# Kernel tuning notes

Measured on AMD Instinct MI355X. Metric: run time of the kernel, lower is better.

Reference implementation:

```python
import jax, jax.numpy as jnp
import numpy as np

GRID = 12  # sqrt(144), seq_len = 144 fixed by w_g shape


def _relative_position(n: int) -> jnp.ndarray:
    # grid cell centers for an n x n grid, flattened row-major -> (n*n,)
    idx = np.arange(n * n)
    row, col = idx // n, idx % n
    cx = (col + 0.5) / n  # (x_min + x_max)/2 with x_min=col/n, x_max=(col+1)/n
    cy = (row + 0.5) / n
    dx = cx[:, None] - cx[None, :]
    dy = cy[:, None] - cy[None, :]
    ax = np.sign(dx) * 0.5
    ay = np.sign(dy) * 0.5
    dx = np.abs(np.log(np.abs(dx) + 0.5))
    dy = np.abs(np.log(np.abs(dy) + 0.5))
    # cat along leading dim then permute(1,2,0) == stack last-dim in order (dx,dy,ax,ay)
    pos = np.stack([dx, dy, ax, ay], axis=-1).astype(np.float32)  # (S,S,4)
    return jnp.asarray(pos)


def setup_inputs() -> dict:
    key = jax.random.key(0)
    ks = jax.random.split(key, 9)
    B, S, D = 128, GRID * GRID, 1024
    sc = 1.0 / np.sqrt(D)
    return {
        "query": jax.random.normal(ks[0], (B, S, D), jnp.float32),
        "key": jax.random.normal(ks[1], (B, S, D), jnp.float32),
        "value": jax.random.normal(ks[2], (B, S, D), jnp.float32),
        "Wq": jax.random.normal(ks[3], (D, D), jnp.float32) * sc,
        "bq": jnp.zeros((D,), jnp.float32),
        "Wk": jax.random.normal(ks[4], (D, D), jnp.float32) * sc,
        "bk": jnp.zeros((D,), jnp.float32),
        "Wv": jax.random.normal(ks[5], (D, D), jnp.float32) * sc,
        "bv": jnp.zeros((D,), jnp.float32),
        "Wlin": jax.random.normal(ks[6], (D, 4), jnp.float32) * 0.5,
        "w_g": jax.random.normal(ks[7], (S, D, 1), jnp.float32) * sc,
    }


def reference(query, key, value, Wq, bq, Wk, bk, Wv, bv, Wlin, w_g):
    d_model = query.shape[-1]
    # QKV projections + ReLU activation (dropout is identity at eval)
    q = jax.nn.relu(jnp.einsum("bsd,ed->bse", query, Wq) + bq)
    k = jax.nn.relu(jnp.einsum("bsd,ed->bse", key, Wk) + bk)
    v = jax.nn.relu(jnp.einsum("bsd,ed->bse", value, Wv) + bv)
    # raw scores: (B, S, S)
    att = jnp.einsum("bsd,btd->bst", q, k) * (d_model ** -0.5)
    # relative-position bias: (S, S, 4) -> linear -> relu -> per-row w_g -> relu
    pos = _relative_position(GRID)
    rp = jax.nn.relu(jnp.einsum("stf,df->std", pos, Wlin))  # (S, S, D)
    rp = jax.nn.relu(jnp.einsum("std,sdo->sto", rp, w_g)[..., 0])  # (S, S)
    att = jax.nn.softmax(att + rp[None, :, :], axis=-1)
    return jnp.einsum("bst,btd->bsd", att, v)
```

## Files before the change

### kernel.cpp

```cpp
#include <hip/hip_runtime.h>
#include <hip/hip_fp16.h>

#define DEV __device__ __forceinline__

using half8 = __attribute__((ext_vector_type(8))) _Float16;
using half4 = __attribute__((ext_vector_type(4))) _Float16;
using f32x4 = __attribute__((ext_vector_type(4))) float;

DEV void gload_lds16(const void* g, void* l) {
  __builtin_amdgcn_global_load_lds((const __attribute__((address_space(1))) unsigned int*)g,
                                   (__attribute__((address_space(3))) unsigned int*)l,
                                   16, 0, 0);
}

DEV f32x4 mfma16x32(half8 a, half8 b, f32x4 c) {
  return __builtin_amdgcn_mfma_f32_16x16x32_f16(a, b, c, 0, 0, 0);
}

DEV void conv2048(const float* __restrict__ s, _Float16* __restrict__ d, int t) {
  int i = t * 8;
  float4 a = *(const float4*)(s + i);
  float4 b = *(const float4*)(s + i + 4);
  half8 h;
  h[0] = (_Float16)a.x; h[1] = (_Float16)a.y; h[2] = (_Float16)a.z; h[3] = (_Float16)a.w;
  h[4] = (_Float16)b.x; h[5] = (_Float16)b.y; h[6] = (_Float16)b.z; h[7] = (_Float16)b.w;
  *(half8*)(d + i) = h;
}

DEV void rp_body(const float* __restrict__ Wlin, const float* __restrict__ wg,
                 float* __restrict__ rp, int s, int t) {
  if (t >= 144) return;
  int rs = s / 12, cs = s % 12, rt = t / 12, ct = t % 12;
  float dx = (cs - ct) / 12.f, dy = (rs - rt) / 12.f;
  float ax = (dx > 0.f) ? 0.5f : (dx < 0.f ? -0.5f : 0.f);
  float ay = (dy > 0.f) ? 0.5f : (dy < 0.f ? -0.5f : 0.f);
  float lx = fabsf(logf(fabsf(dx) + 0.5f));
  float ly = fabsf(logf(fabsf(dy) + 0.5f));
  float a0 = 0.f, a1 = 0.f, a2 = 0.f, a3 = 0.f;
  const float* wgs = wg + s * 1024;
  for (int d = 0; d < 1024; d += 4) {
#pragma unroll
    for (int u = 0; u < 4; ++u) {
      float4 w = *(const float4*)(Wlin + (d + u) * 4);
      float dot = lx * w.x + ly * w.y + ax * w.z + ay * w.w;
      dot = dot > 0.f ? dot : 0.f;
      float p = dot * wgs[d + u];
      if (u == 0) a0 += p; else if (u == 1) a1 += p; else if (u == 2) a2 += p; else a3 += p;
    }
  }
  float acc = (a0 + a1) + (a2 + a3);
  rp[s * 144 + t] = acc > 0.f ? acc : 0.f;
}

__global__ void prep_all(const float* __restrict__ query, const float* __restrict__ key,
                         const float* __restrict__ value, _Float16* __restrict__ ia,
                         _Float16* __restrict__ ib, _Float16* __restrict__ ic,
                         const float* __restrict__ Wq, const float* __restrict__ Wk,
                         const float* __restrict__ Wv, _Float16* __restrict__ Wqb,
                         _Float16* __restrict__ Wkb, _Float16* __restrict__ Wvb,
                         const float* __restrict__ Wlin, const float* __restrict__ wg,
                         float* __restrict__ rp, _Float16* __restrict__ vt) {
  int id = blockIdx.x, t = threadIdx.x;
  if (id < 144) {
    rp_body(Wlin, wg, rp, id, t);
  } else if (id < 656) {
    int i = (id - 144) * 256 + t;
    _Float16* p = vt + (size_t)i * 160 + 144;
    *(half8*)p = (half8){};
    *(half8*)(p + 8) = (half8){};
  } else if (id < 2192) {
    int id3 = id - 656;
    int z = id3 >> 9, r = id3 & 511;
    const float* s = z == 0 ? Wq : (z == 1 ? Wk : Wv);
    _Float16* d = z == 0 ? Wqb : (z == 1 ? Wkb : Wvb);
    conv2048(s + r * 2048, d + r * 2048, t);
  } else {
    int id4 = id - 2192;
    int z = id4 / 9216, r = id4 % 9216;
    const float* s = z == 0 ? query : (z == 1 ? key : value);
    _Float16* d = z == 0 ? ia : (z == 1 ? ib : ic);
    conv2048(s + (size_t)r * 2048, d + (size_t)r * 2048, t);
  }
}

__global__ void prep_small(const float* __restrict__ Wq, const float* __restrict__ Wk,
                           const float* __restrict__ Wv, _Float16* __restrict__ Wqb,
                           _Float16* __restrict__ Wkb, _Float16* __restrict__ Wvb,
                           const float* __restrict__ Wlin, const float* __restrict__ wg,
                           float* __restrict__ rp, _Float16* __restrict__ vt) {
  int id = blockIdx.x, t = threadIdx.x;
  if (id < 144) {
    rp_body(Wlin, wg, rp, id, t);
  } else if (id < 656) {
    int i = (id - 144) * 256 + t;
    _Float16* p = vt + (size_t)i * 160 + 144;
    *(half8*)p = (half8){};
    *(half8*)(p + 8) = (half8){};
  } else {
    int id3 = id - 656;
    int z = id3 >> 9, r = id3 & 511;
    const float* s = z == 0 ? Wq : (z == 1 ? Wk : Wv);
    _Float16* d = z == 0 ? Wqb : (z == 1 ? Wkb : Wvb);
    conv2048(s + r * 2048, d + r * 2048, t);
  }
}

__global__ void conv3_f32_f16(const float* __restrict__ s0, const float* __restrict__ s1,
                              const float* __restrict__ s2, _Float16* __restrict__ d0,
                              _Float16* __restrict__ d1, _Float16* __restrict__ d2, int n) {
  const float* s = blockIdx.z == 0 ? s0 : (blockIdx.z == 1 ? s1 : s2);
  _Float16* d = blockIdx.z == 0 ? d0 : (blockIdx.z == 1 ? d1 : d2);
  int i = blockIdx.x * 2048;
  if (i >= n) return;
  conv2048(s + i, d + i, (int)threadIdx.x);
}

__global__ __launch_bounds__(256, 2) void gemm_proj(
    const _Float16* __restrict__ a0q, const _Float16* __restrict__ a1q,
    const _Float16* __restrict__ a2q, const _Float16* __restrict__ w0q,
    const _Float16* __restrict__ w1q, const _Float16* __restrict__ w2q,
    const float* __restrict__ bi0, const float* __restrict__ bi1,
    const float* __restrict__ bi2, _Float16* __restrict__ c0q,
    _Float16* __restrict__ c1q, _Float16* __restrict__ c2q,
    _Float16* __restrict__ vtp, int vtz) {
  const _Float16* A = blockIdx.z == 0 ? a0q : (blockIdx.z == 1 ? a1q : a2q);
  const _Float16* W = blockIdx.z == 0 ? w0q : (blockIdx.z == 1 ? w1q : w2q);
  const float* bias = blockIdx.z == 0 ? bi0 : (blockIdx.z == 1 ? bi1 : bi2);
  _Float16* C = blockIdx.z == 0 ? c0q : (blockIdx.z == 1 ? c1q : c2q);

  __shared__ __align__(16) char lds[79872];
  int tid = threadIdx.x, wid = tid >> 6, lane = tid & 63;
  int lin = blockIdx.y * 8 + blockIdx.x;
  int local = lin >> 3;
  int mt = (lin & 7) * 8 + (local >> 3), nt = local & 7;
  int m0 = mt * 288, n0 = nt * 128;

  int r4l = lane >> 2, c4 = lane & 3;
  int cg8 = ((c4 + (r4l >> 1)) & 3) * 8;
  int lr = lane & 15, lg = lane >> 4;
  int rdoff = lr * 64 + ((lg - (lr >> 1)) & 3) * 16;

  const _Float16* gp[7];
  int nch = (wid < 2) ? 7 : 6;
#pragma unroll
  for (int c = 0; c < 7; ++c) {
    int q = c * 4 + wid;
    if (q < 26)
      gp[c] = (q < 18) ? A + (size_t)(m0 + q * 16 + r4l) * 1024 + cg8
                       : W + (size_t)(n0 + (q - 18) * 16 + r4l) * 1024 + cg8;
    else
      gp[c] = A;
  }
  char *sl0 = lds, *sl1 = lds + 26624, *sl2 = lds + 53248;
  auto issue = [&](char* slot) {
#pragma unroll
    for (int c = 0; c < 7; ++c) {
      if (c * 4 + wid < 26) { gload_lds16(gp[c], slot + (c * 4 + wid) * 1024); gp[c] += 32; }
    }
  };
  issue(sl0);
  issue(sl1);
  f32x4 acc[9][4] = {};
  int abase = (wid >> 1) * 9216, bbase = 18432 + (wid & 1) * 4096;
  for (int t = 0; t < 32; ++t) {
    if (wid < 2) asm volatile("s_waitcnt vmcnt(7)" ::: "memory");
    else         asm volatile("s_waitcnt vmcnt(6)" ::: "memory");
    __builtin_amdgcn_s_barrier();
    __builtin_amdgcn_sched_barrier(0);
    issue(sl2);
    half8 a[9], b[4];
#pragma unroll
    for (int i = 0; i < 9; ++i) a[i] = *(const half8*)(sl0 + abase + i * 1024 + rdoff);
#pragma unroll
    for (int j = 0; j < 4; ++j) b[j] = *(const half8*)(sl0 + bbase + j * 1024 + rdoff);
#pragma unroll
    for (int i = 0; i < 9; ++i)
#pragma unroll
      for (int j = 0; j < 4; ++j)
        acc[i][j] = mfma16x32(b[j], a[i], acc[i][j]);
    char* tmp = sl0; sl0 = sl1; sl1 = sl2; sl2 = tmp;
  }
  int wm = (wid >> 1) * 144, wn = (wid & 1) * 64;
  bool tov = (vtp != nullptr) && ((int)blockIdx.z == vtz);
#pragma unroll
  for (int i = 0; i < 9; ++i) {
    int row = m0 + wm + i * 16 + lr;
#pragma unroll
    for (int j = 0; j < 4; ++j) {
      int col = n0 + wn + j * 16 + lg * 4;
      float4 b4 = *(const float4*)(bias + col);
      half4 h;
      float v0 = acc[i][j][0] + b4.x; h[0] = (_Float16)(v0 > 0.f ? v0 : 0.f);
      float v1 = acc[i][j][1] + b4.y; h[1] = (_Float16)(v1 > 0.f ? v1 : 0.f);
      float v2 = acc[i][j][2] + b4.z; h[2] = (_Float16)(v2 > 0.f ? v2 : 0.f);
      float v3 = acc[i][j][3] + b4.w; h[3] = (_Float16)(v3 > 0.f ? v3 : 0.f);
      if (tov) {
        int bb = row / 144, ss = row - bb * 144;
        _Float16* vb = vtp + (size_t)(bb * 1024 + col) * 160 + ss;
        vb[0] = h[0]; vb[160] = h[1]; vb[320] = h[2]; vb[480] = h[3];
      } else {
        *(half4*)(C + (size_t)row * 1024 + col) = h;
      }
    }
  }
}

__global__ __launch_bounds__(256) void attn_kernel(const _Float16* __restrict__ q,
                                                   const _Float16* __restrict__ k,
                                                   const _Float16* __restrict__ vt,
                                                   const float* __restrict__ rp,
                                                   float* __restrict__ out) {
  __shared__ __align__(16) char lds[53248];
  float* sc = (float*)lds;
  _Float16* P = (_Float16*)(lds + 36864);
  float* sums = (float*)(lds + 52992);

  int tid = threadIdx.x, wid = tid >> 6, lane = tid & 63;
  int lin = blockIdx.y * 3 + blockIdx.x;
  int swz = (lin & 7) * 48 + (lin >> 3);
  int mt3 = swz % 3, b = swz / 3;
  int m0 = mt3 * 48;
  const int nstart_t[4] = {0, 3, 5, 7};
  const int ncnt_t[4]   = {3, 2, 2, 2};
  int ns = nstart_t[wid], nc = ncnt_t[wid];
  int r4l = lane >> 2, c4 = lane & 3;
  int cg8 = ((c4 + (r4l >> 1)) & 3) * 8;
  int lr = lane & 15, lg = lane >> 4;
  int rdoff = lr * 64 + ((lg - (lr >> 1)) & 3) * 16;

  {
    char *sl0 = lds, *sl1 = lds + 12288, *sl2 = lds + 24576;
    const _Float16* g1[3];
#pragma unroll
    for (int c = 0; c < 3; ++c) {
      int qq = c * 4 + wid;
      g1[c] = (qq < 3) ? q + (size_t)(b * 144 + m0 + qq * 16 + r4l) * 1024 + cg8
                       : k + (size_t)(b * 144 + (qq - 3) * 16 + r4l) * 1024 + cg8;
    }
    auto issue1 = [&](char* slot) {
#pragma unroll
      for (int c = 0; c < 3; ++c) {
        gload_lds16(g1[c], slot + (c * 4 + wid) * 1024);
        g1[c] += 32;
      }
    };
    issue1(sl0);
    issue1(sl1);
    f32x4 acc[3][3] = {};
    for (int t = 0; t < 32; ++t) {
      asm volatile("s_waitcnt vmcnt(3)" ::: "memory");
      __builtin_amdgcn_sched_barrier(0);
      __builtin_amdgcn_s_barrier();
      __builtin_amdgcn_sched_barrier(0);
      issue1(sl2);
      half8 af[3], bf[3];
#pragma unroll
      for (int i = 0; i < 3; ++i)
        af[i] = *(const half8*)(sl0 + i * 1024 + rdoff);
#pragma unroll
      for (int j = 0; j < 3; ++j)
        if (j < nc)
          bf[j] = *(const half8*)(sl0 + (3 + ns + j) * 1024 + rdoff);
#pragma unroll
      for (int i = 0; i < 3; ++i)
#pragma unroll
        for (int j = 0; j < 3; ++j)
          if (j < nc)
            acc[i][j] = mfma16x32(bf[j], af[i], acc[i][j]);
      char* tmp = sl0; sl0 = sl1; sl1 = sl2; sl2 = tmp;
    }
    asm volatile("s_waitcnt vmcnt(0)" ::: "memory");
    __syncthreads();
    const float scale = 0.03125f;
#pragma unroll
    for (int i = 0; i < 3; ++i) {
      int qrow = i * 16 + lr;
#pragma unroll
      for (int j = 0; j < 3; ++j)
        if (j < nc) {
          int kc0 = (ns + j) * 16 + lg * 4;
          float4 rr = *(const float4*)(rp + (m0 + qrow) * 144 + kc0);
          f32x4 vs;
          vs[0] = acc[i][j][0] * scale + rr.x;
          vs[1] = acc[i][j][1] * scale + rr.y;
          vs[2] = acc[i][j][2] * scale + rr.z;
          vs[3] = acc[i][j][3] * scale + rr.w;
          *(f32x4*)(sc + qrow * 152 + kc0) = vs;
        }
    }
  }
  __syncthreads();

  if (tid < 192) {
    int r = tid >> 2, qd = tid & 3;
    int cb = qd * 36;
    float m = -1e30f;
    for (int c2 = 0; c2 < 36; ++c2) m = fmaxf(m, sc[r * 152 + cb + c2]);
    m = fmaxf(m, __shfl_xor(m, 1));
    m = fmaxf(m, __shfl_xor(m, 2));
    float s = 0.f;
    for (int c2 = 0; c2 < 36; ++c2) {
      float e = __expf(sc[r * 152 + cb + c2] - m);
      s += e;
      P[r * 168 + cb + c2] = (_Float16)e;
    }
    s += __shfl_xor(s, 1);
    s += __shfl_xor(s, 2);
    if (qd == 0) sums[r] = s;
  }
  if (tid < 96) {
    int r = tid >> 1, c0 = 144 + (tid & 1) * 8;
    *(half8*)(P + r * 168 + c0) = (half8){};
  }
  __syncthreads();

  char *s0p = lds, *s1p = lds + 16384;
  auto issue2 = [&](int idx, char* slot) {
    int nn0 = (idx / 5) * 256, kk0 = (idx % 5) * 32;
#pragma unroll
    for (int c = 0; c < 4; ++c) {
      int ch = c * 4 + wid;
      gload_lds16(vt + (size_t)(b * 1024 + nn0 + ch * 16 + r4l) * 160 + kk0 + cg8,
                  slot + ch * 1024);
    }
  };
  issue2(0, s0p);
  f32x4 o[3][4] = {};
  for (int it = 0; it < 20; ++it) {
    asm volatile("s_waitcnt vmcnt(0)" ::: "memory");
    __builtin_amdgcn_sched_barrier(0);
    __builtin_amdgcn_s_barrier();
    __builtin_amdgcn_sched_barrier(0);
    issue2(it + 1, ((it + 1) & 1) ? s1p : s0p);
    char* sb = (it & 1) ? s1p : s0p;
    int k0 = (it % 5) * 32;
    half8 af[3], bf[4];
#pragma unroll
    for (int i = 0; i < 3; ++i)
      af[i] = *(const half8*)(P + (i * 16 + lr) * 168 + k0 + lg * 8);
#pragma unroll
    for (int j = 0; j < 4; ++j)
      bf[j] = *(const half8*)(sb + (wid * 4 + j) * 1024 + rdoff);
#pragma unroll
    for (int i = 0; i < 3; ++i)
#pragma unroll
      for (int j = 0; j < 4; ++j)
        o[i][j] = mfma16x32(bf[j], af[i], o[i][j]);
    if (it % 5 == 4) {
      int n0 = (it / 5) * 256;
#pragma unroll
      for (int i = 0; i < 3; ++i) {
        int row = i * 16 + lr;
        float inv = 1.f / sums[row];
#pragma unroll
        for (int j = 0; j < 4; ++j) {
          f32x4 vo;
          vo[0] = o[i][j][0] * inv; vo[1] = o[i][j][1] * inv;
          vo[2] = o[i][j][2] * inv; vo[3] = o[i][j][3] * inv;
          *(f32x4*)(out + (size_t)(b * 144 + m0 + row) * 1024 + n0 + wid * 64 + j * 16 + lg * 4) = vo;
          o[i][j] = (f32x4){};
        }
      }
    }
  }
}

extern "C" void kernel_launch(void* const* d_in, const int* in_sizes, int n_in,
                              void* d_out, int out_size, void* d_ws, size_t ws_size,
                              hipStream_t stream) {
  const float* query = (const float*)d_in[0];
  const float* key   = (const float*)d_in[1];
  const float* value = (const float*)d_in[2];
  const float* Wq    = (const float*)d_in[3];
  const float* bq    = (const float*)d_in[4];
  const float* Wk    = (const float*)d_in[5];
  const float* bk    = (const float*)d_in[6];
  const float* Wv    = (const float*)d_in[7];
  const float* bv    = (const float*)d_in[8];
  const float* Wlin  = (const float*)d_in[9];
  const float* wg    = (const float*)d_in[10];
  float* out = (float*)d_out;

  char* ws = (char*)d_ws;
  const size_t NQKV = (size_t)18432 * 1024;
  const size_t NVT  = (size_t)131072 * 160;
  _Float16* Wqb = (_Float16*)(ws);
  _Float16* Wkb = (_Float16*)(ws + (2u << 20));
  _Float16* Wvb = (_Float16*)(ws + (4u << 20));
  float*    rp  = (float*)(ws + (6u << 20));
  _Float16* qp  = (_Float16*)(ws + (6u << 20) + 131072);
  _Float16* kp  = qp + NQKV;
  _Float16* vt  = kp + NQKV;

  dim3 agrid(3, 128);

  if (ws_size >= 238000000ull) {
    _Float16* ia = vt + NVT + 32768;
    _Float16* ib = ia + NQKV;
    _Float16* ic = ib + NQKV;
    prep_all<<<29840, 256, 0, stream>>>(query, key, value, ia, ib, ic,
                                        Wq, Wk, Wv, Wqb, Wkb, Wvb,
                                        Wlin, wg, rp, vt);
    gemm_proj<<<dim3(8, 64, 3), 256, 0, stream>>>(ia, ib, ic, Wqb, Wkb, Wvb,
                                                  bq, bk, bv, qp, kp, kp ,
                                                  vt, 2);
    attn_kernel<<<agrid, 256, 0, stream>>>(qp, kp, vt, rp, out);
  } else {
    _Float16* inb = vt + NVT;
    prep_small<<<2192, 256, 0, stream>>>(Wq, Wk, Wv, Wqb, Wkb, Wvb, Wlin, wg, rp, vt);
    conv3_f32_f16<<<dim3((int)(NQKV / 2048), 1, 1), 256, 0, stream>>>(
        query, query, query, inb, inb, inb, (int)NQKV);
    gemm_proj<<<dim3(8, 64, 1), 256, 0, stream>>>(inb, inb, inb, Wqb, Wqb, Wqb,
                                                  bq, bq, bq, qp, qp, qp, nullptr, -1);
    conv3_f32_f16<<<dim3((int)(NQKV / 2048), 1, 1), 256, 0, stream>>>(
        key, key, key, inb, inb, inb, (int)NQKV);
    gemm_proj<<<dim3(8, 64, 1), 256, 0, stream>>>(inb, inb, inb, Wkb, Wkb, Wkb,
                                                  bk, bk, bk, kp, kp, kp, nullptr, -1);
    conv3_f32_f16<<<dim3((int)(NQKV / 2048), 1, 1), 256, 0, stream>>>(
        value, value, value, inb, inb, inb, (int)NQKV);
    gemm_proj<<<dim3(8, 64, 1), 256, 0, stream>>>(inb, inb, inb, Wvb, Wvb, Wvb,
                                                  bv, bv, bv, qp , qp, qp,
                                                  vt, 0);
    attn_kernel<<<agrid, 256, 0, stream>>>(qp, kp, vt, rp, out);
  }
}
```

Before: 277.3 us.

## Split attention into score/softmax kernel and parallel PV kernel

Splits the attention kernel in two. The first kernel computes scores and softmax, then writes unnormalized probabilities and row sums to workspace. A second kernel with four times as many blocks computes P·V, each block covering a 256-column slice of the output, so the PV phase gets more parallelism than the old 384-block kernel that looped over all 1024 columns. The cost is an extra launch and a global round trip for P, which is now read straight from global memory rather than LDS.

```diff
diff --git a/kernel.cpp b/kernel.cpp
--- a/kernel.cpp
+++ b/kernel.cpp
@@ -141,7 +141,6 @@
   int rdoff = lr * 64 + ((lg - (lr >> 1)) & 3) * 16;
 
   const _Float16* gp[7];
-  int nch = (wid < 2) ? 7 : 6;
 #pragma unroll
   for (int c = 0; c < 7; ++c) {
     int q = c * 4 + wid;
@@ -205,11 +204,11 @@
   }
 }
 
-__global__ __launch_bounds__(256) void attn_kernel(const _Float16* __restrict__ q,
-                                                   const _Float16* __restrict__ k,
-                                                   const _Float16* __restrict__ vt,
-                                                   const float* __restrict__ rp,
-                                                   float* __restrict__ out) {
+__global__ __launch_bounds__(256) void attn1_kernel(const _Float16* __restrict__ q,
+                                                    const _Float16* __restrict__ k,
+                                                    const float* __restrict__ rp,
+                                                    _Float16* __restrict__ Pg,
+                                                    float* __restrict__ sums_g) {
   __shared__ __align__(16) char lds[53248];
   float* sc = (float*)lds;
   _Float16* P = (_Float16*)(lds + 36864);
@@ -314,30 +313,55 @@
   }
   __syncthreads();
 
+  {
+    int bt = b * 3 + mt3;
+    _Float16* Pgb = Pg + (size_t)bt * 48 * 160;
+    for (int idx = tid; idx < 960; idx += 256) {
+      int r = idx / 20, c = idx % 20;
+      *(half8*)(Pgb + r * 160 + c * 8) = *(const half8*)(P + r * 168 + c * 8);
+    }
+    if (tid < 48) sums_g[bt * 48 + tid] = sums[tid];
+  }
+}
+
+__global__ __launch_bounds__(256) void attn_pv(const _Float16* __restrict__ Pg,
+                                               const float* __restrict__ sums_g,
+                                               const _Float16* __restrict__ vt,
+                                               float* __restrict__ out) {
+  __shared__ __align__(16) char lds[32768];
+  int tid = threadIdx.x, wid = tid >> 6, lane = tid & 63;
+  int lin = blockIdx.y * 12 + blockIdx.x;
+  int swz = (lin & 7) * 192 + (lin >> 3);
+  int bt = swz >> 2, nq = swz & 3;
+  int b = bt / 3, m0 = (bt % 3) * 48;
+  int r4l = lane >> 2, c4 = lane & 3;
+  int cg8 = ((c4 + (r4l >> 1)) & 3) * 8;
+  int lr = lane & 15, lg = lane >> 4;
+  int rdoff = lr * 64 + ((lg - (lr >> 1)) & 3) * 16;
+
   char *s0p = lds, *s1p = lds + 16384;
-  auto issue2 = [&](int idx, char* slot) {
-    int nn0 = (idx / 5) * 256, kk0 = (idx % 5) * 32;
+  auto issue = [&](int it, char* slot) {
 #pragma unroll
     for (int c = 0; c < 4; ++c) {
       int ch = c * 4 + wid;
-      gload_lds16(vt + (size_t)(b * 1024 + nn0 + ch * 16 + r4l) * 160 + kk0 + cg8,
+      gload_lds16(vt + (size_t)(b * 1024 + nq * 256 + ch * 16 + r4l) * 160 + it * 32 + cg8,
                   slot + ch * 1024);
     }
   };
-  issue2(0, s0p);
+  issue(0, s0p);
   f32x4 o[3][4] = {};
-  for (int it = 0; it < 20; ++it) {
+  for (int it = 0; it < 5; ++it) {
     asm volatile("s_waitcnt vmcnt(0)" ::: "memory");
     __builtin_amdgcn_sched_barrier(0);
     __builtin_amdgcn_s_barrier();
     __builtin_amdgcn_sched_barrier(0);
-    issue2(it + 1, ((it + 1) & 1) ? s1p : s0p);
+    if (it < 4) issue(it + 1, (it & 1) ? s0p : s1p);
     char* sb = (it & 1) ? s1p : s0p;
-    int k0 = (it % 5) * 32;
+    int k0 = it * 32;
     half8 af[3], bf[4];
 #pragma unroll
     for (int i = 0; i < 3; ++i)
-      af[i] = *(const half8*)(P + (i * 16 + lr) * 168 + k0 + lg * 8);
+      af[i] = *(const half8*)(Pg + ((size_t)bt * 48 + i * 16 + lr) * 160 + k0 + lg * 8);
 #pragma unroll
     for (int j = 0; j < 4; ++j)
       bf[j] = *(const half8*)(sb + (wid * 4 + j) * 1024 + rdoff);
@@ -346,21 +370,17 @@
 #pragma unroll
       for (int j = 0; j < 4; ++j)
         o[i][j] = mfma16x32(bf[j], af[i], o[i][j]);
-    if (it % 5 == 4) {
-      int n0 = (it / 5) * 256;
-#pragma unroll
-      for (int i = 0; i < 3; ++i) {
-        int row = i * 16 + lr;
-        float inv = 1.f / sums[row];
-#pragma unroll
-        for (int j = 0; j < 4; ++j) {
-          f32x4 vo;
-          vo[0] = o[i][j][0] * inv; vo[1] = o[i][j][1] * inv;
-          vo[2] = o[i][j][2] * inv; vo[3] = o[i][j][3] * inv;
-          *(f32x4*)(out + (size_t)(b * 144 + m0 + row) * 1024 + n0 + wid * 64 + j * 16 + lg * 4) = vo;
-          o[i][j] = (f32x4){};
-        }
-      }
+  }
+#pragma unroll
+  for (int i = 0; i < 3; ++i) {
+    int row = i * 16 + lr;
+    float inv = 1.f / sums_g[bt * 48 + row];
+#pragma unroll
+    for (int j = 0; j < 4; ++j) {
+      f32x4 vo;
+      vo[0] = o[i][j][0] * inv; vo[1] = o[i][j][1] * inv;
+      vo[2] = o[i][j][2] * inv; vo[3] = o[i][j][3] * inv;
+      *(f32x4*)(out + (size_t)(b * 144 + m0 + row) * 1024 + nq * 256 + wid * 64 + j * 16 + lg * 4) = vo;
     }
   }
 }
@@ -392,21 +412,26 @@
   _Float16* kp  = qp + NQKV;
   _Float16* vt  = kp + NQKV;
 
-  dim3 agrid(3, 128);
+  dim3 a1grid(3, 128), pvgrid(12, 128);
 
   if (ws_size >= 238000000ull) {
     _Float16* ia = vt + NVT + 32768;
     _Float16* ib = ia + NQKV;
     _Float16* ic = ib + NQKV;
+    _Float16* Pg = ia;
+    float* sums_g = (float*)((char*)ia + (6u << 20));
     prep_all<<<29840, 256, 0, stream>>>(query, key, value, ia, ib, ic,
                                         Wq, Wk, Wv, Wqb, Wkb, Wvb,
                                         Wlin, wg, rp, vt);
     gemm_proj<<<dim3(8, 64, 3), 256, 0, stream>>>(ia, ib, ic, Wqb, Wkb, Wvb,
                                                   bq, bk, bv, qp, kp, kp ,
                                                   vt, 2);
-    attn_kernel<<<agrid, 256, 0, stream>>>(qp, kp, vt, rp, out);
+    attn1_kernel<<<a1grid, 256, 0, stream>>>(qp, kp, rp, Pg, sums_g);
+    attn_pv<<<pvgrid, 256, 0, stream>>>(Pg, sums_g, vt, out);
   } else {
     _Float16* inb = vt + NVT;
+    _Float16* Pg = inb;
+    float* sums_g = (float*)((char*)inb + (6u << 20));
     prep_small<<<2192, 256, 0, stream>>>(Wq, Wk, Wv, Wqb, Wkb, Wvb, Wlin, wg, rp, vt);
     conv3_f32_f16<<<dim3((int)(NQKV / 2048), 1, 1), 256, 0, stream>>>(
         query, query, query, inb, inb, inb, (int)NQKV);
@@ -421,6 +446,7 @@
     gemm_proj<<<dim3(8, 64, 1), 256, 0, stream>>>(inb, inb, inb, Wvb, Wvb, Wvb,
                                                   bv, bv, bv, qp , qp, qp,
                                                   vt, 0);
-    attn_kernel<<<agrid, 256, 0, stream>>>(qp, kp, vt, rp, out);
-  }
-}
+    attn1_kernel<<<a1grid, 256, 0, stream>>>(qp, kp, rp, Pg, sums_g);
+    attn_pv<<<pvgrid, 256, 0, stream>>>(Pg, sums_g, vt, out);
+  }
+}
```

Measured after the change: 272.5 us. No clear change (-1.7%).
